# Performance work log

Measured on AMD Instinct MI355X. Metric: run time of the kernel, lower is better.

Reference implementation:

```python
import jax, jax.numpy as jnp
import numpy as np
from jax import lax

B, T, FEAT = 8, 512, 128
D_MODEL, D_STATE, D_INNER, DT_RANK = 128, 16, 256, 8
N_LAYERS, NUM_CLASSES = 10, 35
FLAT = 64 * (FEAT // 4)  # 2048


def setup_inputs():
    keys = iter(jax.random.split(jax.random.key(0), 48))
    def nrm(shape, s=0.05):
        return jax.random.normal(next(keys), shape, jnp.float32) * s
    inp = {}
    inp['x'] = jax.random.normal(next(keys), (B, T, FEAT), jnp.float32)
    inp['lengths'] = jax.random.randint(next(keys), (B,), 0, T)
    inp['conv_w1'] = nrm((32, 1, 3, 3)); inp['conv_b1'] = nrm((32,))
    inp['bn1_s'] = 1.0 + nrm((32,)); inp['bn1_b'] = nrm((32,))
    inp['conv_w2'] = nrm((32, 32, 3, 3)); inp['conv_b2'] = nrm((32,))
    inp['bn2_s'] = 1.0 + nrm((32,)); inp['bn2_b'] = nrm((32,))
    inp['conv_w3'] = nrm((64, 32, 3, 3)); inp['conv_b3'] = nrm((64,))
    inp['bn3_s'] = 1.0 + nrm((64,)); inp['bn3_b'] = nrm((64,))
    inp['conv_w4'] = nrm((64, 64, 3, 3)); inp['conv_b4'] = nrm((64,))
    inp['bn4_s'] = 1.0 + nrm((64,)); inp['bn4_b'] = nrm((64,))
    inp['proj_w'] = nrm((D_MODEL, FLAT), 0.02); inp['proj_b'] = nrm((D_MODEL,))
    inp['proj_ln_s'] = jnp.ones((D_MODEL,)); inp['proj_ln_b'] = jnp.zeros((D_MODEL,))
    L = N_LAYERS
    inp['blk_ln_s'] = jnp.ones((L, D_MODEL)); inp['blk_ln_b'] = jnp.zeros((L, D_MODEL))
    inp['in_w'] = nrm((L, 2 * D_INNER, D_MODEL))
    inp['cw'] = nrm((L, D_INNER, 4)); inp['cb'] = nrm((L, D_INNER))
    inp['xp_w'] = nrm((L, DT_RANK + 2 * D_STATE, D_INNER))
    inp['dt_w'] = nrm((L, D_INNER, DT_RANK))
    inp['dt_b'] = nrm((L, D_INNER)) - 4.0  # softplus(-4) ~ 0.018: realistic small dt
    inp['A_log'] = jnp.tile(jnp.log(jnp.arange(1, D_STATE + 1, dtype=jnp.float32))[None, None, :], (L, D_INNER, 1))
    inp['Dp'] = jnp.ones((L, D_INNER))
    inp['out_w'] = nrm((L, D_MODEL, D_INNER))
    inp['pre_ln_s'] = jnp.ones((D_MODEL,)); inp['pre_ln_b'] = jnp.zeros((D_MODEL,))
    inp['cls_w1'] = nrm((D_MODEL // 2, D_MODEL)); inp['cls_b1'] = nrm((D_MODEL // 2,))
    inp['cls_w2'] = nrm((NUM_CLASSES, D_MODEL // 2)); inp['cls_b2'] = nrm((NUM_CLASSES,))
    return inp


def _ln(x, s, b):
    m = jnp.mean(x, -1, keepdims=True)
    v = jnp.mean((x - m) ** 2, -1, keepdims=True)
    return (x - m) * lax.rsqrt(v + 1e-5) * s + b


def _conv2d(x, w, b):
    y = lax.conv_general_dilated(x, w, (1, 1), 'SAME', dimension_numbers=('NCHW', 'OIHW', 'NCHW'))
    return y + b[None, :, None, None]


def _bn(x, s, b):  # eval-mode BatchNorm folded to per-channel affine
    return x * s[None, :, None, None] + b[None, :, None, None]


def _pool(x, kh, kw):
    return lax.reduce_window(x, -jnp.inf, lax.max, (1, 1, kh, kw), (1, 1, kh, kw), 'VALID')


def _mamba(x, in_w, cw, cb, xp_w, dt_w, dt_b, A_log, Dp, out_w):
    bb = x.shape[0]
    xz = jnp.einsum('btd,ed->bte', x, in_w)                  # [B,T,2*d_inner]
    xm, z = jnp.split(xz, 2, axis=-1)
    # causal depthwise conv1d (torch pads both sides by 3 then truncates to T == left-pad 3)
    xc = lax.conv_general_dilated(xm.transpose(0, 2, 1), cw[:, None, :], (1,), [(3, 0)],
                                  dimension_numbers=('NCH', 'OIH', 'NCH'), feature_group_count=D_INNER)
    xc = jax.nn.silu(xc + cb[None, :, None]).transpose(0, 2, 1)  # [B,T,d_inner]
    dbc = jnp.einsum('btd,ed->bte', xc, xp_w)
    dt, Bm, Cm = jnp.split(dbc, [DT_RANK, DT_RANK + D_STATE], axis=-1)
    dt = jax.nn.softplus(jnp.einsum('btr,dr->btd', dt, dt_w) + dt_b)  # [B,T,d_inner]
    A = -jnp.exp(A_log)                                      # [d_inner,d_state]
    dA = jnp.exp(dt[..., None] * A)                          # [B,T,d,n]
    dBu = (dt * xc)[..., None] * Bm[:, :, None, :]           # [B,T,d,n]
    def step(h, inp):
        dA_t, dBu_t, C_t = inp
        h = dA_t * h + dBu_t
        return h, jnp.einsum('bdn,bn->bd', h, C_t)
    h0 = jnp.zeros((bb, D_INNER, D_STATE), x.dtype)
    _, ys = lax.scan(step, h0, (dA.transpose(1, 0, 2, 3), dBu.transpose(1, 0, 2, 3), Cm.transpose(1, 0, 2)))
    y = ys.transpose(1, 0, 2) + Dp * xc
    y = y * jax.nn.silu(z)
    return jnp.einsum('btd,ed->bte', y, out_w)


def _forward(x, lengths, conv_w1, conv_b1, bn1_s, bn1_b, conv_w2, conv_b2, bn2_s, bn2_b,
             conv_w3, conv_b3, bn3_s, bn3_b, conv_w4, conv_b4, bn4_s, bn4_b,
             proj_w, proj_b, proj_ln_s, proj_ln_b, blk_ln_s, blk_ln_b,
             in_w, cw, cb, xp_w, dt_w, dt_b, A_log, Dp, out_w,
             pre_ln_s, pre_ln_b, cls_w1, cls_b1, cls_w2, cls_b2):
    h = x.transpose(0, 2, 1)[:, None]                        # [B,1,F,T]
    h = jax.nn.silu(_bn(_conv2d(h, conv_w1, conv_b1), bn1_s, bn1_b))
    h = jax.nn.silu(_bn(_conv2d(h, conv_w2, conv_b2), bn2_s, bn2_b))
    h = _pool(h, 2, 2)
    h = jax.nn.silu(_bn(_conv2d(h, conv_w3, conv_b3), bn3_s, bn3_b))
    h = jax.nn.silu(_bn(_conv2d(h, conv_w4, conv_b4), bn4_s, bn4_b))
    h = _pool(h, 2, 1)                                       # [B,64,F/4,T/2]
    h = h.transpose(0, 3, 1, 2).reshape(h.shape[0], h.shape[3], -1)  # [B,T',64*F/4]
    h = jax.nn.silu(_ln(jnp.einsum('btf,df->btd', h, proj_w) + proj_b, proj_ln_s, proj_ln_b))
    for i in range(N_LAYERS):
        h = h + _mamba(_ln(h, blk_ln_s[i], blk_ln_b[i]), in_w[i], cw[i], cb[i], xp_w[i],
                       dt_w[i], dt_b[i], A_log[i], Dp[i], out_w[i])
    h = _ln(h, pre_ln_s, pre_ln_b)
    t_lens = jnp.clip(lengths // 2, 1)
    mask = (jnp.arange(h.shape[1])[None, :] < t_lens[:, None]).astype(h.dtype)[..., None]
    pooled = (h * mask).sum(1) / jnp.clip(mask.sum(1), 1.0)
    c = jax.nn.silu(jnp.einsum('bd,hd->bh', pooled, cls_w1) + cls_b1)
    return jnp.einsum('bh,ch->bc', c, cls_w2) + cls_b2


def reference(x, lengths, conv_w1, conv_b1, bn1_s, bn1_b, conv_w2, conv_b2, bn2_s, bn2_b,
              conv_w3, conv_b3, bn3_s, bn3_b, conv_w4, conv_b4, bn4_s, bn4_b,
              proj_w, proj_b, proj_ln_s, proj_ln_b, blk_ln_s, blk_ln_b,
              in_w, cw, cb, xp_w, dt_w, dt_b, A_log, Dp, out_w,
              pre_ln_s, pre_ln_b, cls_w1, cls_b1, cls_w2, cls_b2):
    return _forward(x, lengths, conv_w1, conv_b1, bn1_s, bn1_b, conv_w2, conv_b2, bn2_s, bn2_b,
                    conv_w3, conv_b3, bn3_s, bn3_b, conv_w4, conv_b4, bn4_s, bn4_b,
                    proj_w, proj_b, proj_ln_s, proj_ln_b, blk_ln_s, blk_ln_b,
                    in_w, cw, cb, xp_w, dt_w, dt_b, A_log, Dp, out_w,
                    pre_ln_s, pre_ln_b, cls_w1, cls_b1, cls_w2, cls_b2)
```

## Files before the change

### kernel.cpp

```cpp
#include <hip/hip_runtime.h>
#include <math.h>

#define B_ 8
#define T_ 512
#define FEAT_ 128
#define TP 256
#define DM 128
#define DI 256
#define DS 16
#define DTR 8
#define NL 10

typedef _Float16 h2 __attribute__((ext_vector_type(2)));
typedef unsigned int uint32;

__device__ __forceinline__ float fsilu(float x){ return x / (1.f + __expf(-x)); }
__device__ __forceinline__ float fsoftplus(float x){ return (x > 20.f) ? x : log1pf(__expf(x)); }

__device__ __forceinline__ uint32 pack_h2(float a, float b){
  union { h2 h; uint32 u; } cv;
  cv.h[0] = (_Float16)a; cv.h[1] = (_Float16)b;
  return cv.u;
}
__device__ __forceinline__ h2 as_h2(uint32 u){
  union { uint32 u; h2 h; } cv; cv.u = u; return cv.h;
}

template<int CTRL>
__device__ __forceinline__ float dpp_ror(float x){
  int v = __builtin_amdgcn_update_dpp(0, __float_as_int(x), CTRL, 0xF, 0xF, false);
  return __int_as_float(v);
}
__device__ __forceinline__ float rsum16(float x){
  x += dpp_ror<0x121>(x);
  x += dpp_ror<0x122>(x);
  x += dpp_ror<0x124>(x);
  x += dpp_ror<0x128>(x);
  return x;
}

__global__ void k_transpose_x(const float* __restrict__ x, float* __restrict__ xT){
  int idx = blockIdx.x*256 + threadIdx.x;
  if(idx >= B_*FEAT_*T_) return;
  int t = idx % T_; int f = (idx/T_) % FEAT_; int b = idx/(T_*FEAT_);
  xT[idx] = x[((size_t)b*T_ + t)*FEAT_ + f];
}

__device__ __forceinline__ void wt_one(const float* __restrict__ w, float* __restrict__ o,
                                       int idx, int CO, int CIN){
  int k = idx % 9; int ci = (idx/9) % CIN; int co = idx/(9*CIN);
  o[((size_t)(ci*(CO>>3) + (co>>3)))*72 + (co&7)*9 + k] = w[idx];
}
__device__ __forceinline__ void wt_pack(const float* __restrict__ w, uint32* __restrict__ o,
                                        int idx, int CO, int CIN){
  int CIN2 = CIN >> 1;
  int k = idx % 9; int ci2 = (idx/9) % CIN2; int co = idx/(9*CIN2);
  float f0 = w[((size_t)co*CIN + 2*ci2 + 0)*9 + k];
  float f1 = w[((size_t)co*CIN + 2*ci2 + 1)*9 + k];
  o[((size_t)(ci2*(CO>>3) + (co>>3)))*72 + (co&7)*9 + k] = pack_h2(f0, f1);
}
__global__ void k_wt_all(const float* __restrict__ w1, const float* __restrict__ w2,
                         const float* __restrict__ w4,
                         float* __restrict__ o1, uint32* __restrict__ o2,
                         uint32* __restrict__ o4){
  int idx = blockIdx.x*256 + threadIdx.x;
  if(idx < 288){ wt_one(w1, o1, idx, 32, 1); return; }
  idx -= 288;
  if(idx < 4608){ wt_pack(w2, o2, idx, 32, 32); return; }
  idx -= 4608;
  if(idx < 18432){ wt_pack(w4, o4, idx, 64, 64); return; }
}
__global__ void k_wt3(const float* __restrict__ w3, uint32* __restrict__ o3){
  int idx = blockIdx.x*256 + threadIdx.x;
  if(idx < 9216) wt_pack(w3, o3, idx, 64, 32);
}

__global__ void k_pack_w(const float* __restrict__ in_w, const float* __restrict__ out_w,
                         uint32* __restrict__ in_wh, uint32* __restrict__ out_wh){
  int idx = blockIdx.x*256 + threadIdx.x;
  int tot1 = NL*512*64;
  if(idx < tot1){
    const float* w = in_w + (size_t)idx*2;
    in_wh[idx] = pack_h2(w[0], w[1]);
    return;
  }
  idx -= tot1;
  if(idx < NL*128*128){
    const float* w = out_w + (size_t)idx*2;
    out_wh[idx] = pack_h2(w[0], w[1]);
  }
}

template<int CIN, int CO, int CPW, int CIG, int COG>
__global__ __launch_bounds__(256) void k_conv_t4(const float* __restrict__ in,
     const float* __restrict__ wt, const float* __restrict__ cb,
     const float* __restrict__ bs, const float* __restrict__ bb,
     float* __restrict__ out, int H, int W){
  constexpr int NS = CO/CPW;
  __shared__ __align__(16) float tile[CIG*360];
  int tid = threadIdx.x;
  int lane = tid & 63;
  int wav = __builtin_amdgcn_readfirstlane(tid >> 6);
  int wpr = W >> 4, hpr = H >> 4;
  int idx = blockIdx.x;
  int cog = idx % COG; idx /= COG;
  int tj = idx % wpr; idx /= wpr;
  int ti = idx % hpr; int b = idx / hpr;
  int i0 = ti*16, j0 = tj*16;
  int r = lane & 15, cg = lane >> 4;
  int wslot = cog*4 + wav;
  const float* wbase = wt + (size_t)wslot*72;
  float acc[CPW][4] = {};
  for(int cig = 0; cig < CIN; cig += CIG){
    __syncthreads();
    for(int u = tid; u < CIG*324; u += 256){
      int ci = u / 324; int rem = u - ci*324; int rr = rem / 18; int cc = rem - rr*18;
      int gi = i0 - 1 + rr, gj = j0 - 1 + cc;
      float v = 0.f;
      if(gi >= 0 && gi < H && gj >= 0 && gj < W)
        v = in[((size_t)(b*CIN + cig + ci)*H + gi)*W + gj];
      tile[ci*360 + rr*20 + cc] = v;
    }
    __syncthreads();
    for(int ci = 0; ci < CIG; ci++){
      const float4* wp4 = (const float4*)(wbase + (size_t)(cig+ci)*(NS*72));
      float4 w4q[18];
      #pragma unroll
      for(int q=0;q<18;q++) w4q[q] = wp4[q];
      const float* wf = (const float*)w4q;
      #pragma unroll
      for(int kh=0;kh<3;kh++){
        float4 a = *(const float4*)&tile[ci*360 + (r+kh)*20 + cg*4];
        float4 bv = *(const float4*)&tile[ci*360 + (r+kh)*20 + cg*4 + 4];
        float v[6] = {a.x,a.y,a.z,a.w,bv.x,bv.y};
        #pragma unroll
        for(int co=0;co<CPW;co++){
          #pragma unroll
          for(int kw=0;kw<3;kw++){
            float wv = wf[co*9 + kh*3 + kw];
            #pragma unroll
            for(int u2=0;u2<4;u2++)
              acc[co][u2] = fmaf(wv, v[kw+u2], acc[co][u2]);
          }
        }
      }
    }
  }
  int i = i0 + r;
  #pragma unroll
  for(int co=0; co<CPW; co++){
    int c = cog*(4*CPW) + wav*CPW + co;
    float s = bs[c], bias = cb[c]*s + bb[c];
    float4 o;
    o.x = fsilu(acc[co][0]*s + bias);
    o.y = fsilu(acc[co][1]*s + bias);
    o.z = fsilu(acc[co][2]*s + bias);
    o.w = fsilu(acc[co][3]*s + bias);
    *(float4*)&out[((size_t)(b*CO + c)*H + i)*W + j0 + cg*4] = o;
  }
}

template<int CIN2, int CO, int CPW, int CIG2, int COG>
__global__ __launch_bounds__(256) void k_conv_t7(const float* __restrict__ in,
     const uint32* __restrict__ wt, const float* __restrict__ cb,
     const float* __restrict__ bs, const float* __restrict__ bb,
     float* __restrict__ out, int H, int W){
  constexpr int NS = CO/CPW;
  constexpr int NSLAB = CIN2/CIG2;
  constexpr int NEL = CIG2*324;
  constexpr int NLD = (NEL + 255)/256;
  __shared__ __align__(16) uint32 tile[CIG2*360];
  int tid = threadIdx.x;
  int lane = tid & 63;
  int wav = __builtin_amdgcn_readfirstlane(tid >> 6);
  int wpr = W >> 4, hpr = H >> 4;
  int idx = blockIdx.x;
  int cog = idx % COG; idx /= COG;
  int tj = idx % wpr; idx /= wpr;
  int ti = idx % hpr; int b = idx / hpr;
  int i0 = ti*16, j0 = tj*16;
  int r = lane & 15, cg = lane >> 4;
  int wslot = cog*4 + wav;
  const uint32* wbase = wt + (size_t)wslot*72;
  float acc[CPW][4] = {};
  float r0[NLD], r1[NLD];

  auto LOAD = [&](int c2g){
    #pragma unroll
    for(int l=0;l<NLD;l++){
      int u = tid + l*256;
      float v0 = 0.f, v1 = 0.f;
      if(u < NEL){
        int ci2 = u/324; int rem = u - ci2*324; int rr = rem/18; int cc = rem - rr*18;
        int gi = i0 - 1 + rr, gj = j0 - 1 + cc;
        if(gi >= 0 && gi < H && gj >= 0 && gj < W){
          const float* p = in + ((size_t)(b*(CIN2*2) + (c2g+ci2)*2)*H + gi)*W + gj;
          v0 = p[0];
          v1 = p[(size_t)H*W];
        }
      }
      r0[l] = v0; r1[l] = v1;
    }
  };
  auto WRITE = [&](){
    #pragma unroll
    for(int l=0;l<NLD;l++){
      int u = tid + l*256;
      if(u < NEL){
        int ci2 = u/324; int rem = u - ci2*324; int rr = rem/18; int cc = rem - rr*18;
        tile[ci2*360 + rr*20 + cc] = pack_h2(r0[l], r1[l]);
      }
    }
  };

  LOAD(0);
  for(int s=0; s<NSLAB; s++){
    __syncthreads();
    WRITE();
    __syncthreads();
    if(s+1 < NSLAB) LOAD((s+1)*CIG2);
    #pragma unroll
    for(int ci2=0; ci2<CIG2; ci2++){
      int sci2 = s*CIG2 + ci2;
      const uint4* wp4 = (const uint4*)(wbase + (size_t)sci2*(NS*72));
      uint4 w4q[18];
      #pragma unroll
      for(int q=0;q<18;q++) w4q[q] = wp4[q];
      const uint32* wf = (const uint32*)w4q;
      h2 v[3][6];
      #pragma unroll
      for(int kh=0;kh<3;kh++){
        const uint32* trow = &tile[ci2*360 + (r+kh)*20 + cg*4];
        uint4 a4 = *(const uint4*)trow;
        v[kh][0]=as_h2(a4.x); v[kh][1]=as_h2(a4.y);
        v[kh][2]=as_h2(a4.z); v[kh][3]=as_h2(a4.w);
        v[kh][4]=as_h2(trow[4]); v[kh][5]=as_h2(trow[5]);
      }
      #pragma unroll
      for(int co=0;co<CPW;co++){
        #pragma unroll
        for(int kh=0;kh<3;kh++){
          #pragma unroll
          for(int kw=0;kw<3;kw++){
            h2 wv = as_h2(wf[co*9 + kh*3 + kw]);
            #pragma unroll
            for(int u2=0;u2<4;u2++)
              acc[co][u2] = __builtin_amdgcn_fdot2(wv, v[kh][kw+u2], acc[co][u2], false);
          }
        }
      }
    }
  }
  int i = i0 + r;
  #pragma unroll
  for(int co=0; co<CPW; co++){
    int c = cog*(4*CPW) + wav*CPW + co;
    float s = bs[c], bias = cb[c]*s + bb[c];
    float4 o;
    o.x = fsilu(acc[co][0]*s + bias);
    o.y = fsilu(acc[co][1]*s + bias);
    o.z = fsilu(acc[co][2]*s + bias);
    o.w = fsilu(acc[co][3]*s + bias);
    *(float4*)&out[((size_t)(b*CO + c)*H + i)*W + j0 + cg*4] = o;
  }
}

__global__ void k_pool2x2(const float* __restrict__ in, float* __restrict__ out,
                          int C, int Hi, int Wi){
  int Ho = Hi>>1, Wo = Wi>>1;
  int total = B_*C*Ho*Wo;
  int idx = blockIdx.x*256 + threadIdx.x;
  if(idx >= total) return;
  int j = idx % Wo; int i = (idx/Wo)%Ho; int c = (idx/(Wo*Ho))%C; int b = idx/(Wo*Ho*C);
  const float* p = in + (((size_t)(b*C+c)*Hi + 2*i)*Wi + 2*j);
  out[idx] = fmaxf(fmaxf(p[0], p[1]), fmaxf(p[Wi], p[Wi+1]));
}

__global__ __launch_bounds__(256) void k_proj(const float* __restrict__ R0,
    const float* __restrict__ W, float* __restrict__ pbuf){
  __shared__ __align__(16) float As[16][33];
  __shared__ __align__(16) float Ws[16][68];
  int tid = threadIdx.x;
  int n0 = blockIdx.x*64, m0 = blockIdx.y*32;
  int kc = blockIdx.z;
  int b = m0 >> 8;
  int t_base = m0 & 255;
  int tx = tid&15, ty = tid>>4;
  float acc[2][4] = {};
  for(int k0=0; k0<256; k0+=16){
    int kg0 = kc*256 + k0;
    if(tid < 128){
      int row = tid>>2, cq = (tid&3)*4;
      #pragma unroll
      for(int c2=0;c2<4;c2++){
        int k = kg0 + cq + c2;
        int c = k>>5, hh = k&31;
        const float* p = R0 + (((size_t)(b*64+c)*64 + 2*hh)*256 + t_base + row);
        As[cq+c2][row] = fmaxf(p[0], p[256]);
      }
    } else {
      int u = tid - 128; int n = u>>1, cq = (u&1)*8;
      const float* wp = W + (size_t)(n0+n)*2048 + kg0 + cq;
      float4 v0 = *(const float4*)wp, v1 = *(const float4*)(wp+4);
      Ws[cq+0][n]=v0.x; Ws[cq+1][n]=v0.y; Ws[cq+2][n]=v0.z; Ws[cq+3][n]=v0.w;
      Ws[cq+4][n]=v1.x; Ws[cq+5][n]=v1.y; Ws[cq+6][n]=v1.z; Ws[cq+7][n]=v1.w;
    }
    __syncthreads();
    #pragma unroll
    for(int kk=0;kk<16;kk++){
      float a0 = As[kk][ty*2+0];
      float a1 = As[kk][ty*2+1];
      float4 w4 = *(const float4*)&Ws[kk][tx*4];
      float wv4[4] = {w4.x,w4.y,w4.z,w4.w};
      #pragma unroll
      for(int j=0;j<4;j++){
        acc[0][j] = fmaf(a0, wv4[j], acc[0][j]);
        acc[1][j] = fmaf(a1, wv4[j], acc[1][j]);
      }
    }
    __syncthreads();
  }
  float* pb = pbuf + (size_t)kc*2048*DM;
  #pragma unroll
  for(int iu=0;iu<2;iu++){
    int m = m0 + ty*2 + iu;
    #pragma unroll
    for(int j=0;j<4;j++){
      int n = n0 + tx*4 + j;
      pb[(size_t)m*DM + n] = acc[iu][j];
    }
  }
}

__global__ void k_lnp(const float* __restrict__ pbuf, const float* __restrict__ bias,
                      const float* __restrict__ g, const float* __restrict__ b,
                      float* __restrict__ out){
  int row = blockIdx.x;
  int t = threadIdx.x;
  float v0 = bias[t], v1 = bias[t+64];
  #pragma unroll
  for(int kc=0;kc<8;kc++){
    const float* p = pbuf + ((size_t)kc*2048 + row)*DM;
    v0 += p[t]; v1 += p[t+64];
  }
  float s = v0 + v1;
  #pragma unroll
  for(int m=32;m>=1;m>>=1) s += __shfl_xor(s, m);
  float mean = s * (1.f/128.f);
  float e0 = v0-mean, e1 = v1-mean;
  float q = e0*e0 + e1*e1;
  #pragma unroll
  for(int m=32;m>=1;m>>=1) q += __shfl_xor(q, m);
  float inv = rsqrtf(q*(1.f/128.f) + 1e-5f);
  float o0 = fsilu(e0*inv*g[t] + b[t]);
  float o1 = fsilu(e1*inv*g[t+64] + b[t+64]);
  float* po = out + (size_t)row*DM;
  po[t] = o0; po[t+64] = o1;
}

__global__ __launch_bounds__(256) void k_lnxz2(const float* __restrict__ hbuf,
    const float* __restrict__ g, const float* __restrict__ bb,
    const uint32* __restrict__ Wh, float* __restrict__ out){
  __shared__ __align__(16) float lns[32][132];
  __shared__ __align__(16) uint32 ah[32][68];
  __shared__ __align__(16) uint32 wsh[8][68];
  int tid = threadIdx.x;
  int n0 = blockIdx.x*64, m0 = blockIdx.y*32;
  for(int u=tid; u<1024; u+=256){
    int row = u>>5, c4 = (u&31)*4;
    float4 v = *(const float4*)(hbuf + (size_t)(m0+row)*DM + c4);
    lns[row][c4] = v.x; lns[row][c4+1] = v.y; lns[row][c4+2] = v.z; lns[row][c4+3] = v.w;
  }
  __syncthreads();
  {
    int lane = tid & 63, wv = tid >> 6;
    for(int rr = wv; rr < 32; rr += 4){
      float v0 = lns[rr][lane], v1 = lns[rr][lane+64];
      float s = v0+v1;
      #pragma unroll
      for(int mm=32;mm>=1;mm>>=1) s += __shfl_xor(s,mm);
      float mean = s*(1.f/128.f);
      float e0 = v0-mean, e1 = v1-mean;
      float q = e0*e0+e1*e1;
      #pragma unroll
      for(int mm=32;mm>=1;mm>>=1) q += __shfl_xor(q,mm);
      float inv = rsqrtf(q*(1.f/128.f)+1e-5f);
      lns[rr][lane]    = e0*inv*g[lane] + bb[lane];
      lns[rr][lane+64] = e1*inv*g[lane+64] + bb[lane+64];
    }
  }
  __syncthreads();
  for(int u=tid; u<32*64; u+=256){
    int row = u>>6, p = u&63;
    ah[row][p] = pack_h2(lns[row][2*p], lns[row][2*p+1]);
  }
  __syncthreads();
  int tx = tid&15, ty = tid>>4;
  float acc[2][4] = {};
  for(int kp0=0; kp0<64; kp0+=8){
    {
      int n = tid>>2, c = (tid&3)*2;
      uint2 v = *(const uint2*)(Wh + (size_t)(n0+n)*64 + kp0 + c);
      wsh[c+0][n] = v.x; wsh[c+1][n] = v.y;
    }
    __syncthreads();
    #pragma unroll
    for(int kp=0;kp<8;kp++){
      h2 a0 = as_h2(ah[ty*2+0][kp0+kp]);
      h2 a1 = as_h2(ah[ty*2+1][kp0+kp]);
      uint4 w4 = *(const uint4*)&wsh[kp][tx*4];
      acc[0][0] = __builtin_amdgcn_fdot2(a0, as_h2(w4.x), acc[0][0], false);
      acc[0][1] = __builtin_amdgcn_fdot2(a0, as_h2(w4.y), acc[0][1], false);
      acc[0][2] = __builtin_amdgcn_fdot2(a0, as_h2(w4.z), acc[0][2], false);
      acc[0][3] = __builtin_amdgcn_fdot2(a0, as_h2(w4.w), acc[0][3], false);
      acc[1][0] = __builtin_amdgcn_fdot2(a1, as_h2(w4.x), acc[1][0], false);
      acc[1][1] = __builtin_amdgcn_fdot2(a1, as_h2(w4.y), acc[1][1], false);
      acc[1][2] = __builtin_amdgcn_fdot2(a1, as_h2(w4.z), acc[1][2], false);
      acc[1][3] = __builtin_amdgcn_fdot2(a1, as_h2(w4.w), acc[1][3], false);
    }
    __syncthreads();
  }
  #pragma unroll
  for(int iu=0;iu<2;iu++){
    int m = m0 + ty*2 + iu;
    float* po = out + (size_t)m*512 + n0 + tx*4;
    #pragma unroll
    for(int j=0;j<4;j++) po[j] = acc[iu][j];
  }
}

__global__ __launch_bounds__(256) void k_xproj8(const float* __restrict__ xz,
    const float* __restrict__ cw, const float* __restrict__ cb,
    const float* __restrict__ xpw, const float* __restrict__ dtw,
    const float* __restrict__ dtb_, float* __restrict__ xc_g,
    float* __restrict__ dbc_g, float* __restrict__ dt_g){
  __shared__ float xzs[11][64];
  __shared__ float As[64][9];
  __shared__ float Wp[64][41];
  __shared__ float dtin[8][9];
  __shared__ float dtw_s[256][9];
  int tid = threadIdx.x;
  int row0 = blockIdx.x*8; int b = row0 >> 8; int t0 = row0 & 255;
  int rA = tid & 7, cgA = tid >> 3;
  int dlC = tid & 63, rqC = tid >> 6;
  float acc0 = 0.f, acc1 = 0.f;
  for(int ch=0; ch<4; ch++){
    int d0 = ch*64;
    __syncthreads();
    for(int u=tid; u<11*64; u+=256){
      int rr = u>>6, dl = u&63;
      int t = t0 + rr - 3;
      xzs[rr][dl] = (t >= 0) ? xz[((size_t)(b*TP)+t)*512 + d0 + dl] : 0.f;
    }
    for(int u=tid; u<40*64; u+=256){
      int nn = u>>6, dk = u&63;
      Wp[dk][nn] = xpw[(size_t)nn*DI + d0 + dk];
    }
    __syncthreads();
    {
      float cw0 = cw[(d0+dlC)*4+0], cw1 = cw[(d0+dlC)*4+1];
      float cw2 = cw[(d0+dlC)*4+2], cw3 = cw[(d0+dlC)*4+3];
      float cbv = cb[d0+dlC];
      #pragma unroll
      for(int i=0;i<2;i++){
        int rr = rqC*2 + i;
        float a = cbv;
        a = fmaf(cw0, xzs[rr+0][dlC], a);
        a = fmaf(cw1, xzs[rr+1][dlC], a);
        a = fmaf(cw2, xzs[rr+2][dlC], a);
        a = fmaf(cw3, xzs[rr+3][dlC], a);
        float v = fsilu(a);
        As[dlC][rr] = v;
        xc_g[((size_t)row0 + rr)*DI + d0 + dlC] = v;
      }
    }
    __syncthreads();
    for(int dk=0; dk<64; dk++){
      float a = As[dk][rA];
      acc0 = fmaf(a, Wp[dk][cgA], acc0);
      if(cgA < 8) acc1 = fmaf(a, Wp[dk][cgA+32], acc1);
    }
  }
  if(cgA < 8){
    dtin[rA][cgA] = acc0;
    dbc_g[((size_t)row0 + rA)*40 + cgA + 32] = acc1;
  } else {
    dbc_g[((size_t)row0 + rA)*40 + cgA] = acc0;
  }
  for(int u=tid; u<256*8; u+=256) dtw_s[u>>3][u&7] = dtw[u];
  __syncthreads();
  {
    int d = tid;
    float bias = dtb_[d];
    float w8[8];
    #pragma unroll
    for(int k=0;k<8;k++) w8[k] = dtw_s[d][k];
    #pragma unroll
    for(int r2=0;r2<8;r2++){
      float a = bias;
      #pragma unroll
      for(int k=0;k<8;k++) a = fmaf(dtin[r2][k], w8[k], a);
      dt_g[((size_t)row0 + r2)*DI + d] = fsoftplus(a);
    }
  }
}

__global__ __launch_bounds__(1024) void k_scan4(const float* __restrict__ dtb,
      const float* __restrict__ xc, const float* __restrict__ xz,
      const float* __restrict__ dbc, const float* __restrict__ A_log,
      const float* __restrict__ Dp, float* __restrict__ y){
  __shared__ float dt_s[TP][8], xc_s[TP][8];
  __shared__ float Bs[TP][16], Cs[TP][16];
  __shared__ float Eb[8][128], Pb[8][128];
  int tid = threadIdx.x;
  int c = tid >> 7, gl = (tid >> 4) & 7, n = tid & 15;
  int dblk = blockIdx.x & 31, b = blockIdx.x >> 5;
  int d0 = dblk*8;
  size_t rbase = (size_t)b*TP;
  for(int u=tid; u<TP*8; u+=1024){
    int tt = u>>3, gg = u&7;
    size_t r = rbase + tt;
    dt_s[tt][gg] = dtb[r*DI + d0 + gg];
    xc_s[tt][gg] = xc [r*DI + d0 + gg];
  }
  for(int u=tid; u<TP*16; u+=1024){
    int tt = u>>4, nn = u&15;
    size_t r = rbase + tt;
    Bs[tt][nn] = dbc[r*40 + 8  + nn];
    Cs[tt][nn] = dbc[r*40 + 24 + nn];
  }
  __syncthreads();
  int d = d0 + gl;
  float An = -__expf(A_log[d*DS + n]);
  float h = 0.f, dtsum = 0.f;
  int tA = c*32;
  float hc[32], ev[32];
  #pragma unroll
  for(int i=0;i<32;i++){
    int t = tA + i;
    float dtv = dt_s[t][gl];
    dtsum += dtv;
    float e = __expf(dtv*An);
    ev[i] = e;
    h = fmaf(e, h, dtv*xc_s[t][gl]*Bs[t][n]);
    hc[i] = h*Cs[t][n];
  }
  Eb[c][gl*16+n] = h;
  Pb[c][gl*16+n] = __expf(An*dtsum);
  __syncthreads();
  float g = 0.f;
  for(int cp=0; cp<c; cp++)
    g = fmaf(Pb[cp][gl*16+n], g, Eb[cp][gl*16+n]);
  float Dpd = Dp[d];
  #pragma unroll
  for(int i=0;i<32;i++){
    int t = tA + i;
    g *= ev[i];
    float p = rsum16(hc[i] + g*Cs[t][n]);
    if(n==0){
      float zv = xz[(rbase+t)*512 + DI + d];
      float xcv = xc_s[t][gl];
      y[(rbase+t)*DI + d] = (p + Dpd*xcv) * fsilu(zv);
    }
  }
}

__global__ __launch_bounds__(256) void k_out16h(const float* __restrict__ A,
    const uint32* __restrict__ Wh, float* __restrict__ C){
  __shared__ __align__(16) uint32 As2[8][20];
  __shared__ __align__(16) uint32 wsh[8][68];
  int tid = threadIdx.x;
  int n0 = blockIdx.x*64, m0 = blockIdx.y*16;
  int tx = tid&15, ty = tid>>4;
  float acc[4] = {};
  for(int kp0=0; kp0<128; kp0+=8){
    if(tid < 128){
      int row = tid>>3, kp = tid&7;
      float2 v = *(const float2*)(A + (size_t)(m0+row)*DI + (kp0+kp)*2);
      As2[kp][row] = pack_h2(v.x, v.y);
    } else {
      int u = tid-128; int n = u>>1, c4 = (u&1)*4;
      uint4 v = *(const uint4*)(Wh + (size_t)(n0+n)*128 + kp0 + c4);
      wsh[c4+0][n]=v.x; wsh[c4+1][n]=v.y; wsh[c4+2][n]=v.z; wsh[c4+3][n]=v.w;
    }
    __syncthreads();
    #pragma unroll
    for(int kp=0;kp<8;kp++){
      h2 a = as_h2(As2[kp][ty]);
      uint4 w4 = *(const uint4*)&wsh[kp][tx*4];
      acc[0] = __builtin_amdgcn_fdot2(a, as_h2(w4.x), acc[0], false);
      acc[1] = __builtin_amdgcn_fdot2(a, as_h2(w4.y), acc[1], false);
      acc[2] = __builtin_amdgcn_fdot2(a, as_h2(w4.z), acc[2], false);
      acc[3] = __builtin_amdgcn_fdot2(a, as_h2(w4.w), acc[3], false);
    }
    __syncthreads();
  }
  int m = m0 + ty;
  float* cp = &C[(size_t)m*DM + n0 + tx*4];
  cp[0] += acc[0]; cp[1] += acc[1]; cp[2] += acc[2]; cp[3] += acc[3];
}

__global__ __launch_bounds__(256) void k_head2(const float* __restrict__ h,
    const int* __restrict__ lengths, const float* __restrict__ g,
    const float* __restrict__ bv, const float* __restrict__ w1,
    const float* __restrict__ b1, const float* __restrict__ w2,
    const float* __restrict__ b2, float* __restrict__ out){
  __shared__ float pp[4][128];
  __shared__ float pooled[DM];
  __shared__ float cbuf[64];
  int b = blockIdx.x, tid = threadIdx.x;
  int lane = tid & 63, wv = tid >> 6;
  int tl = lengths[b] >> 1; if(tl < 1) tl = 1;
  float p0 = 0.f, p1 = 0.f;
  for(int t = wv; t < tl; t += 4){
    const float* row = h + ((size_t)(b*TP)+t)*DM;
    float v0 = row[lane], v1 = row[lane+64];
    float s = v0+v1;
    #pragma unroll
    for(int mm=32;mm>=1;mm>>=1) s += __shfl_xor(s,mm);
    float mean = s*(1.f/128.f);
    float e0 = v0-mean, e1 = v1-mean;
    float q = e0*e0+e1*e1;
    #pragma unroll
    for(int mm=32;mm>=1;mm>>=1) q += __shfl_xor(q,mm);
    float inv = rsqrtf(q*(1.f/128.f)+1e-5f);
    p0 += e0*inv*g[lane] + bv[lane];
    p1 += e1*inv*g[lane+64] + bv[lane+64];
  }
  pp[wv][lane] = p0; pp[wv][lane+64] = p1;
  __syncthreads();
  if(tid < 128)
    pooled[tid] = (pp[0][tid]+pp[1][tid]+pp[2][tid]+pp[3][tid]) / (float)tl;
  __syncthreads();
  if(tid < 64){
    float a = b1[tid];
    const float* wp = w1 + tid*DM;
    for(int k=0;k<DM;k++) a = fmaf(pooled[k], wp[k], a);
    cbuf[tid] = fsilu(a);
  }
  __syncthreads();
  if(tid < 35){
    float a = b2[tid];
    const float* wp = w2 + tid*64;
    for(int k=0;k<64;k++) a = fmaf(cbuf[k], wp[k], a);
    out[b*35+tid] = a;
  }
}

extern "C" void kernel_launch(void* const* d_in, const int* in_sizes, int n_in,
                              void* d_out, int out_size, void* d_ws, size_t ws_size,
                              hipStream_t stream){
  (void)in_sizes; (void)n_in; (void)out_size; (void)ws_size;
  const float* x        = (const float*)d_in[0];
  const int*   lengths  = (const int*)  d_in[1];
  const float* conv_w1  = (const float*)d_in[2];  const float* conv_b1 = (const float*)d_in[3];
  const float* bn1_s    = (const float*)d_in[4];  const float* bn1_b   = (const float*)d_in[5];
  const float* conv_w2  = (const float*)d_in[6];  const float* conv_b2 = (const float*)d_in[7];
  const float* bn2_s    = (const float*)d_in[8];  const float* bn2_b   = (const float*)d_in[9];
  const float* conv_w3  = (const float*)d_in[10]; const float* conv_b3 = (const float*)d_in[11];
  const float* bn3_s    = (const float*)d_in[12]; const float* bn3_b   = (const float*)d_in[13];
  const float* conv_w4  = (const float*)d_in[14]; const float* conv_b4 = (const float*)d_in[15];
  const float* bn4_s    = (const float*)d_in[16]; const float* bn4_b   = (const float*)d_in[17];
  const float* proj_w   = (const float*)d_in[18]; const float* proj_b  = (const float*)d_in[19];
  const float* proj_ln_s= (const float*)d_in[20]; const float* proj_ln_b=(const float*)d_in[21];
  const float* blk_ln_s = (const float*)d_in[22]; const float* blk_ln_b =(const float*)d_in[23];
  const float* in_w     = (const float*)d_in[24];
  const float* cw       = (const float*)d_in[25]; const float* cbv     = (const float*)d_in[26];
  const float* xp_w     = (const float*)d_in[27];
  const float* dt_w     = (const float*)d_in[28]; const float* dt_b    = (const float*)d_in[29];
  const float* A_log    = (const float*)d_in[30]; const float* Dp      = (const float*)d_in[31];
  const float* out_w    = (const float*)d_in[32];
  const float* pre_ln_s = (const float*)d_in[33]; const float* pre_ln_b= (const float*)d_in[34];
  const float* cls_w1   = (const float*)d_in[35]; const float* cls_b1  = (const float*)d_in[36];
  const float* cls_w2   = (const float*)d_in[37]; const float* cls_b2  = (const float*)d_in[38];

  float* ws   = (float*)d_ws;
  float* R0   = ws;
  float* R1   = R0 + 16777216;
  float* xT   = R1 + 16777216;
  float* hbuf = xT + 524288;
  float* lnb  = hbuf + 262144;
  float* xzb  = lnb + 262144;
  float* xcb  = xzb + 1048576;
  float* dbcb = xcb + 524288;
  float* dtbb = dbcb + 81920;
  float* yb   = dtbb + 524288;
  float* wt1  = yb + 524288;
  uint32* wt2h = (uint32*)(wt1 + 288);
  uint32* wt3h = wt2h + 4608;
  uint32* wt4h = wt3h + 9216;
  uint32* in_wh  = wt4h + 18432;
  uint32* out_wh = in_wh + 327680;

  k_wt_all<<<96, 256, 0, stream>>>(conv_w1, conv_w2, conv_w4, wt1, wt2h, wt4h);
  k_wt3<<<36, 256, 0, stream>>>(conv_w3, wt3h);
  k_pack_w<<<1920, 256, 0, stream>>>(in_w, out_w, in_wh, out_wh);

  k_transpose_x<<<2048, 256, 0, stream>>>(x, xT);
  k_conv_t4<1,32,8,1,1><<<8*8*32, 256, 0, stream>>>(xT, wt1, conv_b1, bn1_s, bn1_b, R0, 128, 512);
  k_conv_t7<16,32,8,8,1><<<8*8*32, 256, 0, stream>>>(R0, wt2h, conv_b2, bn2_s, bn2_b, R1, 128, 512);
  k_pool2x2<<<(8*32*64*256)/256, 256, 0, stream>>>(R1, R0, 32, 128, 512);
  k_conv_t7<16,64,8,8,2><<<8*4*16*2, 256, 0, stream>>>(R0, wt3h, conv_b3, bn3_s, bn3_b, R1, 64, 256);
  k_conv_t7<32,64,8,8,2><<<8*4*16*2, 256, 0, stream>>>(R1, wt4h, conv_b4, bn4_s, bn4_b, R0, 64, 256);

  {
    dim3 gd(2, 64, 8);
    k_proj<<<gd, 256, 0, stream>>>(R0, proj_w, R1);
  }
  k_lnp<<<2048, 64, 0, stream>>>(R1, proj_b, proj_ln_s, proj_ln_b, hbuf);

  for(int i=0;i<NL;i++){
    { dim3 gd(8, 64);
      k_lnxz2<<<gd, 256, 0, stream>>>(hbuf, blk_ln_s + i*DM, blk_ln_b + i*DM,
                                      in_wh + (size_t)i*512*64, xzb); }
    k_xproj8<<<256, 256, 0, stream>>>(xzb, cw + (size_t)i*DI*4, cbv + i*DI,
                                      xp_w + (size_t)i*40*DI, dt_w + (size_t)i*DI*DTR,
                                      dt_b + i*DI, xcb, dbcb, dtbb);
    k_scan4<<<256, 1024, 0, stream>>>(dtbb, xcb, xzb, dbcb, A_log + (size_t)i*DI*DS, Dp + i*DI, yb);
    { dim3 gd(2, 128);
      k_out16h<<<gd, 256, 0, stream>>>(yb, out_wh + (size_t)i*128*128, hbuf); }
  }

  k_head2<<<8, 256, 0, stream>>>(hbuf, lengths, pre_ln_s, pre_ln_b,
                                 cls_w1, cls_b1, cls_w2, cls_b2, (float*)d_out);
}
```

Baseline: 1.106 ms.

## Fuse out-projection residual with next layer's LayerNorm and in-projection

```diff
diff --git a/kernel.cpp b/kernel.cpp
--- a/kernel.cpp
+++ b/kernel.cpp
@@ -426,6 +426,117 @@
     float* po = out + (size_t)m*512 + n0 + tx*4;
     #pragma unroll
     for(int j=0;j<4;j++) po[j] = acc[iu][j];
+  }
+}
+
+__global__ __launch_bounds__(256) void k_blk(const float* __restrict__ y,
+    const uint32* __restrict__ Wout, float* __restrict__ hb,
+    const float* __restrict__ g, const float* __restrict__ bb,
+    const uint32* __restrict__ Wxz, float* __restrict__ xz){
+  __shared__ __align__(16) float hrow[16][132];
+  __shared__ __align__(16) uint32 ypk[128][18];
+  __shared__ __align__(16) uint32 wstg[4352];
+  __shared__ __align__(16) uint32 ah[16][66];
+  int tid = threadIdx.x;
+  int m0 = blockIdx.x*16;
+  int ty = tid>>4, tx = tid&15;
+  for(int u=tid; u<512; u+=256){
+    int row = u>>5, c4 = (u&31)*4;
+    float4 v = *(const float4*)(hb + (size_t)(m0+row)*DM + c4);
+    hrow[row][c4]=v.x; hrow[row][c4+1]=v.y; hrow[row][c4+2]=v.z; hrow[row][c4+3]=v.w;
+  }
+  for(int u=tid; u<1024; u+=256){
+    int row = u>>6, kp2 = (u&63)*2;
+    float4 v = *(const float4*)(y + (size_t)(m0+row)*DI + 2*kp2);
+    ypk[kp2][row]   = pack_h2(v.x, v.y);
+    ypk[kp2+1][row] = pack_h2(v.z, v.w);
+  }
+  float acc[8] = {};
+  for(int kp0=0; kp0<128; kp0+=8){
+    __syncthreads();
+    {
+      int n = tid>>1, kq = (tid&1)*4;
+      uint4 v = *(const uint4*)(Wout + (size_t)n*128 + kp0 + kq);
+      wstg[(kq+0)*132+n]=v.x; wstg[(kq+1)*132+n]=v.y;
+      wstg[(kq+2)*132+n]=v.z; wstg[(kq+3)*132+n]=v.w;
+    }
+    __syncthreads();
+    #pragma unroll
+    for(int kp=0;kp<8;kp++){
+      h2 a = as_h2(ypk[kp0+kp][ty]);
+      const uint32* wp = &wstg[kp*132 + tx*8];
+      uint4 wA = *(const uint4*)wp;
+      uint4 wB = *(const uint4*)(wp+4);
+      acc[0] = __builtin_amdgcn_fdot2(a, as_h2(wA.x), acc[0], false);
+      acc[1] = __builtin_amdgcn_fdot2(a, as_h2(wA.y), acc[1], false);
+      acc[2] = __builtin_amdgcn_fdot2(a, as_h2(wA.z), acc[2], false);
+      acc[3] = __builtin_amdgcn_fdot2(a, as_h2(wA.w), acc[3], false);
+      acc[4] = __builtin_amdgcn_fdot2(a, as_h2(wB.x), acc[4], false);
+      acc[5] = __builtin_amdgcn_fdot2(a, as_h2(wB.y), acc[5], false);
+      acc[6] = __builtin_amdgcn_fdot2(a, as_h2(wB.z), acc[6], false);
+      acc[7] = __builtin_amdgcn_fdot2(a, as_h2(wB.w), acc[7], false);
+    }
+  }
+  float hv[8];
+  #pragma unroll
+  for(int j=0;j<8;j++){
+    hv[j] = hrow[ty][tx*8+j] + acc[j];
+    hrow[ty][tx*8+j] = hv[j];
+  }
+  {
+    float* po = hb + (size_t)(m0+ty)*DM + tx*8;
+    float4 o0 = {hv[0],hv[1],hv[2],hv[3]};
+    float4 o1 = {hv[4],hv[5],hv[6],hv[7]};
+    *(float4*)po = o0; *(float4*)(po+4) = o1;
+  }
+  __syncthreads();
+  {
+    int lane = tid & 63, wv = tid >> 6;
+    for(int rr = wv; rr < 16; rr += 4){
+      float v0 = hrow[rr][lane], v1 = hrow[rr][lane+64];
+      float s = v0+v1;
+      #pragma unroll
+      for(int mm=32;mm>=1;mm>>=1) s += __shfl_xor(s,mm);
+      float mean = s*(1.f/128.f);
+      float e0 = v0-mean, e1 = v1-mean;
+      float q = e0*e0+e1*e1;
+      #pragma unroll
+      for(int mm=32;mm>=1;mm>>=1) q += __shfl_xor(q,mm);
+      float inv = rsqrtf(q*(1.f/128.f)+1e-5f);
+      hrow[rr][lane]    = e0*inv*g[lane] + bb[lane];
+      hrow[rr][lane+64] = e1*inv*g[lane+64] + bb[lane+64];
+    }
+  }
+  __syncthreads();
+  for(int u=tid; u<1024; u+=256){
+    int row = u>>6, p = u&63;
+    ah[row][p] = pack_h2(hrow[row][2*p], hrow[row][2*p+1]);
+  }
+  for(int nc=0; nc<8; nc++){
+    __syncthreads();
+    {
+      #pragma unroll
+      for(int l=0;l<4;l++){
+        int u = tid + l*256;
+        int n = u>>4, kq = (u&15)*4;
+        uint4 v = *(const uint4*)(Wxz + (size_t)(nc*64+n)*64 + kq);
+        wstg[(kq+0)*68+n]=v.x; wstg[(kq+1)*68+n]=v.y;
+        wstg[(kq+2)*68+n]=v.z; wstg[(kq+3)*68+n]=v.w;
+      }
+    }
+    __syncthreads();
+    float a2[4] = {};
+    #pragma unroll 8
+    for(int kp=0;kp<64;kp++){
+      h2 a = as_h2(ah[ty][kp]);
+      uint4 w4 = *(const uint4*)&wstg[kp*68 + tx*4];
+      a2[0] = __builtin_amdgcn_fdot2(a, as_h2(w4.x), a2[0], false);
+      a2[1] = __builtin_amdgcn_fdot2(a, as_h2(w4.y), a2[1], false);
+      a2[2] = __builtin_amdgcn_fdot2(a, as_h2(w4.z), a2[2], false);
+      a2[3] = __builtin_amdgcn_fdot2(a, as_h2(w4.w), a2[3], false);
+    }
+    float4 o = {a2[0],a2[1],a2[2],a2[3]};
+    *(float4*)(xz + (size_t)(m0+ty)*512 + nc*64 + tx*4) = o;
   }
 }
 
@@ -709,16 +820,21 @@
   }
   k_lnp<<<2048, 64, 0, stream>>>(R1, proj_b, proj_ln_s, proj_ln_b, hbuf);
 
+  { dim3 gd(8, 64);
+    k_lnxz2<<<gd, 256, 0, stream>>>(hbuf, blk_ln_s, blk_ln_b, in_wh, xzb); }
   for(int i=0;i<NL;i++){
-    { dim3 gd(8, 64);
-      k_lnxz2<<<gd, 256, 0, stream>>>(hbuf, blk_ln_s + i*DM, blk_ln_b + i*DM,
-                                      in_wh + (size_t)i*512*64, xzb); }
     k_xproj8<<<256, 256, 0, stream>>>(xzb, cw + (size_t)i*DI*4, cbv + i*DI,
                                       xp_w + (size_t)i*40*DI, dt_w + (size_t)i*DI*DTR,
                                       dt_b + i*DI, xcb, dbcb, dtbb);
     k_scan4<<<256, 1024, 0, stream>>>(dtbb, xcb, xzb, dbcb, A_log + (size_t)i*DI*DS, Dp + i*DI, yb);
-    { dim3 gd(2, 128);
-      k_out16h<<<gd, 256, 0, stream>>>(yb, out_wh + (size_t)i*128*128, hbuf); }
+    if(i < NL-1){
+      k_blk<<<128, 256, 0, stream>>>(yb, out_wh + (size_t)i*128*128, hbuf,
+                                     blk_ln_s + (i+1)*DM, blk_ln_b + (i+1)*DM,
+                                     in_wh + (size_t)(i+1)*512*64, xzb);
+    } else {
+      dim3 gd(2, 128);
+      k_out16h<<<gd, 256, 0, stream>>>(yb, out_wh + (size_t)i*128*128, hbuf);
+    }
   }
 
   k_head2<<<8, 256, 0, stream>>>(hbuf, lengths, pre_ln_s, pre_ln_b,
```

Result: slower. 1.197 ms (+8.2%).

## Fuse first two conv layers, recomputing conv1 halo tile in shared memory

Applied to the files above, without the earlier changes.

```diff
diff --git a/kernel.cpp b/kernel.cpp
--- a/kernel.cpp
+++ b/kernel.cpp
@@ -46,11 +46,6 @@
   xT[idx] = x[((size_t)b*T_ + t)*FEAT_ + f];
 }
 
-__device__ __forceinline__ void wt_one(const float* __restrict__ w, float* __restrict__ o,
-                                       int idx, int CO, int CIN){
-  int k = idx % 9; int ci = (idx/9) % CIN; int co = idx/(9*CIN);
-  o[((size_t)(ci*(CO>>3) + (co>>3)))*72 + (co&7)*9 + k] = w[idx];
-}
 __device__ __forceinline__ void wt_pack(const float* __restrict__ w, uint32* __restrict__ o,
                                         int idx, int CO, int CIN){
   int CIN2 = CIN >> 1;
@@ -59,13 +54,9 @@
   float f1 = w[((size_t)co*CIN + 2*ci2 + 1)*9 + k];
   o[((size_t)(ci2*(CO>>3) + (co>>3)))*72 + (co&7)*9 + k] = pack_h2(f0, f1);
 }
-__global__ void k_wt_all(const float* __restrict__ w1, const float* __restrict__ w2,
-                         const float* __restrict__ w4,
-                         float* __restrict__ o1, uint32* __restrict__ o2,
-                         uint32* __restrict__ o4){
+__global__ void k_wt_all(const float* __restrict__ w2, const float* __restrict__ w4,
+                         uint32* __restrict__ o2, uint32* __restrict__ o4){
   int idx = blockIdx.x*256 + threadIdx.x;
-  if(idx < 288){ wt_one(w1, o1, idx, 32, 1); return; }
-  idx -= 288;
   if(idx < 4608){ wt_pack(w2, o2, idx, 32, 32); return; }
   idx -= 4608;
   if(idx < 18432){ wt_pack(w4, o4, idx, 64, 64); return; }
@@ -91,72 +82,99 @@
   }
 }
 
-template<int CIN, int CO, int CPW, int CIG, int COG>
-__global__ __launch_bounds__(256) void k_conv_t4(const float* __restrict__ in,
-     const float* __restrict__ wt, const float* __restrict__ cb,
-     const float* __restrict__ bs, const float* __restrict__ bb,
-     float* __restrict__ out, int H, int W){
-  constexpr int NS = CO/CPW;
-  __shared__ __align__(16) float tile[CIG*360];
+__global__ __launch_bounds__(256) void k_conv12(const float* __restrict__ xT,
+     const float* __restrict__ w1, const float* __restrict__ cb1,
+     const float* __restrict__ bs1, const float* __restrict__ bb1,
+     const uint32* __restrict__ wt2, const float* __restrict__ cb2,
+     const float* __restrict__ bs2, const float* __restrict__ bb2,
+     float* __restrict__ out){
+  const int H = 128, W = 512;
+  __shared__ __align__(16) float xin[400];
+  __shared__ __align__(16) uint32 c1pk[16*360];
+  __shared__ float w1s[288];
+  __shared__ float bn1s[32], bn1b[32];
   int tid = threadIdx.x;
   int lane = tid & 63;
   int wav = __builtin_amdgcn_readfirstlane(tid >> 6);
-  int wpr = W >> 4, hpr = H >> 4;
   int idx = blockIdx.x;
-  int cog = idx % COG; idx /= COG;
-  int tj = idx % wpr; idx /= wpr;
-  int ti = idx % hpr; int b = idx / hpr;
+  int tj = idx % 32; idx /= 32;
+  int ti = idx % 8;  int b = idx / 8;
   int i0 = ti*16, j0 = tj*16;
+  for(int u=tid; u<288; u+=256) w1s[u] = w1[u];
+  if(tid < 32){ float s = bs1[tid]; bn1s[tid] = s; bn1b[tid] = cb1[tid]*s + bb1[tid]; }
+  for(int u=tid; u<400; u+=256){
+    int rr = u/20, cc = u - rr*20;
+    int gi = i0 - 2 + rr, gj = j0 - 2 + cc;
+    float v = 0.f;
+    if(gi >= 0 && gi < H && gj >= 0 && gj < W)
+      v = xT[((size_t)b*H + gi)*W + gj];
+    xin[rr*20+cc] = v;
+  }
+  __syncthreads();
+  for(int u=tid; u<324*16; u+=256){
+    int ci2 = u/324; int pos = u - ci2*324; int rr = pos/18, cc = pos - rr*18;
+    int gi = i0 - 1 + rr, gj = j0 - 1 + cc;
+    float v0 = 0.f, v1 = 0.f;
+    if(gi >= 0 && gi < H && gj >= 0 && gj < W){
+      int c0 = 2*ci2, c1 = 2*ci2+1;
+      float a0 = 0.f, a1 = 0.f;
+      #pragma unroll
+      for(int kh=0;kh<3;kh++)
+        #pragma unroll
+        for(int kw=0;kw<3;kw++){
+          float xv = xin[(rr+kh)*20 + cc+kw];
+          a0 = fmaf(w1s[c0*9 + kh*3 + kw], xv, a0);
+          a1 = fmaf(w1s[c1*9 + kh*3 + kw], xv, a1);
+        }
+      v0 = fsilu(a0*bn1s[c0] + bn1b[c0]);
+      v1 = fsilu(a1*bn1s[c1] + bn1b[c1]);
+    }
+    c1pk[ci2*360 + rr*20 + cc] = pack_h2(v0, v1);
+  }
+  __syncthreads();
   int r = lane & 15, cg = lane >> 4;
-  int wslot = cog*4 + wav;
-  const float* wbase = wt + (size_t)wslot*72;
-  float acc[CPW][4] = {};
-  for(int cig = 0; cig < CIN; cig += CIG){
-    __syncthreads();
-    for(int u = tid; u < CIG*324; u += 256){
-      int ci = u / 324; int rem = u - ci*324; int rr = rem / 18; int cc = rem - rr*18;
-      int gi = i0 - 1 + rr, gj = j0 - 1 + cc;
-      float v = 0.f;
-      if(gi >= 0 && gi < H && gj >= 0 && gj < W)
-        v = in[((size_t)(b*CIN + cig + ci)*H + gi)*W + gj];
-      tile[ci*360 + rr*20 + cc] = v;
-    }
-    __syncthreads();
-    for(int ci = 0; ci < CIG; ci++){
-      const float4* wp4 = (const float4*)(wbase + (size_t)(cig+ci)*(NS*72));
-      float4 w4q[18];
-      #pragma unroll
-      for(int q=0;q<18;q++) w4q[q] = wp4[q];
-      const float* wf = (const float*)w4q;
+  const uint32* wbase = wt2 + (size_t)wav*72;
+  float acc[8][4] = {};
+  for(int ci2=0; ci2<16; ci2++){
+    const uint4* wp4 = (const uint4*)(wbase + (size_t)ci2*(4*72));
+    uint4 w4q[18];
+    #pragma unroll
+    for(int q=0;q<18;q++) w4q[q] = wp4[q];
+    const uint32* wf = (const uint32*)w4q;
+    h2 v[3][6];
+    #pragma unroll
+    for(int kh=0;kh<3;kh++){
+      const uint32* trow = &c1pk[ci2*360 + (r+kh)*20 + cg*4];
+      uint4 a4 = *(const uint4*)trow;
+      v[kh][0]=as_h2(a4.x); v[kh][1]=as_h2(a4.y);
+      v[kh][2]=as_h2(a4.z); v[kh][3]=as_h2(a4.w);
+      v[kh][4]=as_h2(trow[4]); v[kh][5]=as_h2(trow[5]);
+    }
+    #pragma unroll
+    for(int co=0;co<8;co++){
       #pragma unroll
       for(int kh=0;kh<3;kh++){
-        float4 a = *(const float4*)&tile[ci*360 + (r+kh)*20 + cg*4];
-        float4 bv = *(const float4*)&tile[ci*360 + (r+kh)*20 + cg*4 + 4];
-        float v[6] = {a.x,a.y,a.z,a.w,bv.x,bv.y};
         #pragma unroll
-        for(int co=0;co<CPW;co++){
+        for(int kw=0;kw<3;kw++){
+          h2 wv = as_h2(wf[co*9 + kh*3 + kw]);
           #pragma unroll
-          for(int kw=0;kw<3;kw++){
-            float wv = wf[co*9 + kh*3 + kw];
-            #pragma unroll
-            for(int u2=0;u2<4;u2++)
-              acc[co][u2] = fmaf(wv, v[kw+u2], acc[co][u2]);
-          }
+          for(int u2=0;u2<4;u2++)
+            acc[co][u2] = __builtin_amdgcn_fdot2(wv, v[kh][kw+u2], acc[co][u2], false);
         }
       }
     }
   }
   int i = i0 + r;
   #pragma unroll
-  for(int co=0; co<CPW; co++){
-    int c = cog*(4*CPW) + wav*CPW + co;
-    float s = bs[c], bias = cb[c]*s + bb[c];
+  for(int co=0; co<8; co++){
+    int c = wav*8 + co;
+    float s = bs2[c], bias = cb2[c]*s + bb2[c];
     float4 o;
     o.x = fsilu(acc[co][0]*s + bias);
     o.y = fsilu(acc[co][1]*s + bias);
     o.z = fsilu(acc[co][2]*s + bias);
     o.w = fsilu(acc[co][3]*s + bias);
-    *(float4*)&out[((size_t)(b*CO + c)*H + i)*W + j0 + cg*4] = o;
+    *(float4*)&out[((size_t)(b*32 + c)*H + i)*W + j0 + cg*4] = o;
   }
 }
 
@@ -685,20 +703,19 @@
   float* dbcb = xcb + 524288;
   float* dtbb = dbcb + 81920;
   float* yb   = dtbb + 524288;
-  float* wt1  = yb + 524288;
-  uint32* wt2h = (uint32*)(wt1 + 288);
+  uint32* wt2h = (uint32*)(yb + 524288);
   uint32* wt3h = wt2h + 4608;
   uint32* wt4h = wt3h + 9216;
   uint32* in_wh  = wt4h + 18432;
   uint32* out_wh = in_wh + 327680;
 
-  k_wt_all<<<96, 256, 0, stream>>>(conv_w1, conv_w2, conv_w4, wt1, wt2h, wt4h);
+  k_wt_all<<<90, 256, 0, stream>>>(conv_w2, conv_w4, wt2h, wt4h);
   k_wt3<<<36, 256, 0, stream>>>(conv_w3, wt3h);
   k_pack_w<<<1920, 256, 0, stream>>>(in_w, out_w, in_wh, out_wh);
 
   k_transpose_x<<<2048, 256, 0, stream>>>(x, xT);
-  k_conv_t4<1,32,8,1,1><<<8*8*32, 256, 0, stream>>>(xT, wt1, conv_b1, bn1_s, bn1_b, R0, 128, 512);
-  k_conv_t7<16,32,8,8,1><<<8*8*32, 256, 0, stream>>>(R0, wt2h, conv_b2, bn2_s, bn2_b, R1, 128, 512);
+  k_conv12<<<2048, 256, 0, stream>>>(xT, conv_w1, conv_b1, bn1_s, bn1_b,
+                                     wt2h, conv_b2, bn2_s, bn2_b, R1);
   k_pool2x2<<<(8*32*64*256)/256, 256, 0, stream>>>(R1, R0, 32, 128, 512);
   k_conv_t7<16,64,8,8,2><<<8*4*16*2, 256, 0, stream>>>(R0, wt3h, conv_b3, bn3_s, bn3_b, R1, 64, 256);
   k_conv_t7<32,64,8,8,2><<<8*4*16*2, 256, 0, stream>>>(R1, wt4h, conv_b4, bn4_s, bn4_b, R0, 64, 256);
```

New measurement: 1.098 ms. No clear change (-0.8%).
